# Kernel tuning notes

Measured on AMD Instinct MI355X. Metric: run time of the kernel, lower is better.

## Reference

```python
import jax, jax.numpy as jnp
import numpy as np

N_KNOTS = 10
NEXPERTS = 1
NC = 8
STEP = 1.0 / (N_KNOTS - 1.0)
BN_EPS = 1e-5


def _spline_matrix(n, step):
    # natural cubic spline second-derivative solve matrix (precalc in torch code)
    mat = 4.0 * np.eye(n - 2)
    np.fill_diagonal(mat[1:, :-1], 1.0)
    np.fill_diagonal(mat[:-1, 1:], 1.0)
    A = 6.0 * np.linalg.inv(mat) / step ** 2
    z = np.zeros((1, n - 2))
    A = np.vstack([z, A, z])                      # [n, n-2]
    B = np.zeros((n - 2, n))
    np.fill_diagonal(B, 1.0)
    np.fill_diagonal(B[:, 1:], -2.0)
    np.fill_diagonal(B[:, 2:], 1.0)
    return jnp.asarray(A @ B, dtype=jnp.float32)  # [n, n]


def _conv(x, w, b, stride=2):
    y = jax.lax.conv_general_dilated(x, w, (stride, stride), 'VALID',
                                     dimension_numbers=('NCHW', 'OIHW', 'NCHW'))
    return y + b[None, :, None, None]


def _bn(x, g, be):
    # training-mode batchnorm (module default)
    m = x.mean(axis=(0, 2, 3), keepdims=True)
    v = x.var(axis=(0, 2, 3), keepdims=True)
    return g[None, :, None, None] * (x - m) * jax.lax.rsqrt(v + BN_EPS) + be[None, :, None, None]


def _interpolate(ys, mat):
    # ys: [..., n] -> cubic coeffs a,b,c,d each [..., n-1]
    h = STEP
    M = jnp.einsum('ij,...j->...i', mat, ys)
    a = (M[..., 1:] - M[..., :-1]) / (6.0 * h)
    b = M[..., :-1] / 2.0
    c = (ys[..., 1:] - ys[..., :-1]) / h - (M[..., 1:] + 2.0 * M[..., :-1]) * (h / 6.0)
    d = ys[..., :-1]
    return a, b, c, d


def _apply(coeffs, x):
    # coeffs: 4-tuple each [..., n-1]; x: [..., P] with matching leading dims
    a, b, c, d = coeffs
    xi = jnp.clip(jnp.floor(x / STEP), 0.0, N_KNOTS - 2.0)
    xf = x - xi * STEP
    idx = xi.astype(jnp.int32)
    ag = jnp.take_along_axis(a, idx, axis=-1)
    bg = jnp.take_along_axis(b, idx, axis=-1)
    cg = jnp.take_along_axis(c, idx, axis=-1)
    dg = jnp.take_along_axis(d, idx, axis=-1)
    return ((ag * xf + bg) * xf + cg) * xf + dg


def forward(x, w1, b1, w2, b2, g2, be2, w3, b3, g3, be3, w4, b4, g4, be4,
            w5, b5, g5, be5, fc1_w, fc1_b, fc2_w, fc2_b):
    B, C, H, W = x.shape
    small = x if (H, W) == (256, 256) else jax.image.resize(x, (B, C, 256, 256), 'bilinear')
    h = jax.nn.relu(_conv(small, w1, b1))
    h = _bn(jax.nn.relu(_conv(h, w2, b2)), g2, be2)
    h = _bn(jax.nn.relu(_conv(h, w3, b3)), g3, be3)
    h = _bn(jax.nn.relu(_conv(h, w4, b4)), g4, be4)
    h = _bn(jax.nn.relu(_conv(h, w5, b5)), g5, be5)   # [B, 16nc, 7, 7]
    h = h.mean(axis=(2, 3))                            # avgpool 7 -> [B, 16nc]
    h = jax.nn.relu(h @ fc1_w.T + fc1_b)
    ys = (h @ fc2_w.T + fc2_b).reshape(B, NEXPERTS, 3, N_KNOTS)
    identity = jnp.arange(N_KNOTS, dtype=jnp.float32) / (N_KNOTS - 1.0)
    ysn = ys + identity                                # residual spline
    mat = _spline_matrix(N_KNOTS, STEP)
    coeffs = _interpolate(ysn, mat)                    # each [B,E,3,n-1]
    # per-pixel spline eval at original resolution
    px = jnp.broadcast_to(x.reshape(B, 1, 3, H * W), (B, NEXPERTS, 3, H * W))
    out = _apply(coeffs, px).reshape(B, NEXPERTS, 3, H, W)
    out = jnp.transpose(out, (1, 0, 2, 3, 4))          # [E,B,3,H,W]
    # spline curves sampled at xs = arange(0,1,1/255) (255 points; detached in torch)
    xs = jnp.arange(0.0, 1.0, 1.0 / 255.0, dtype=jnp.float32)
    xs_b = jnp.broadcast_to(xs, (B, NEXPERTS, 3, xs.shape[0]))
    splines = jnp.transpose(_apply(coeffs, xs_b), (1, 0, 2, 3))  # [E,B,3,255]
    return out, splines


def setup_inputs() -> dict:
    key = jax.random.key(0)
    ks = jax.random.split(key, 16)
    n, nc, E = N_KNOTS, NC, NEXPERTS
    d = {}
    d['x'] = jax.random.uniform(ks[0], (8, 3, 1024, 1024), dtype=jnp.float32)
    d['w1'] = jax.random.normal(ks[1], (nc, 3, 3, 3), jnp.float32) * 0.1
    d['b1'] = jnp.zeros((nc,), jnp.float32)
    chans = [nc, 2 * nc, 4 * nc, 8 * nc, 16 * nc]
    for i, (ci, co) in enumerate(zip(chans[:-1], chans[1:]), start=2):
        d[f'w{i}'] = jax.random.normal(ks[i], (co, ci, 3, 3), jnp.float32) * 0.1
        d[f'b{i}'] = jnp.zeros((co,), jnp.float32)
        d[f'g{i}'] = jnp.ones((co,), jnp.float32)
        d[f'be{i}'] = jnp.zeros((co,), jnp.float32)
    d['fc1_w'] = jax.random.normal(ks[10], (16 * nc, 16 * nc), jnp.float32) * 0.05
    d['fc1_b'] = jnp.zeros((16 * nc,), jnp.float32)
    d['fc2_w'] = jax.random.normal(ks[11], (3 * n * E, 16 * nc), jnp.float32) * 0.05
    d['fc2_b'] = jnp.zeros((3 * n * E,), jnp.float32)
    return d


def reference(x, w1, b1, w2, b2, g2, be2, w3, b3, g3, be3, w4, b4, g4, be4,
              w5, b5, g5, be5, fc1_w, fc1_b, fc2_w, fc2_b):
    return forward(x, w1, b1, w2, b2, g2, be2, w3, b3, g3, be3, w4, b4, g4, be4,
                   w5, b5, g5, be5, fc1_w, fc1_b, fc2_w, fc2_b)
```

## Files before the change

### kernel.cpp

```cpp
#include <hip/hip_runtime.h>

#define SPLINE_OFF 25165824
#define STEP_F (1.0f/9.0f)

typedef float f32x4 __attribute__((ext_vector_type(4)));

__global__ __launch_bounds__(256) void resize_k(const float* __restrict__ x,
                                                float* __restrict__ sm,
                                                unsigned* __restrict__ ctr) {
    __shared__ float vs[4][1024];
    const int blk = blockIdx.x;
    const int plane = blk >> 6;
    const int orA = (blk & 63) * 4;
    const int t = threadIdx.x;
    if (blk == 0 && t == 0) ctr[0] = 0u;

    const float W[8] = {0.125f,0.375f,0.625f,0.875f,0.875f,0.625f,0.375f,0.125f};
    const float* p = x + (size_t)plane * 1048576 + t * 4;
    const int rb = 4 * orA - 2;

    float acc[4][4];
    #pragma unroll
    for (int o = 0; o < 4; o++)
        #pragma unroll
        for (int c = 0; c < 4; c++) acc[o][c] = 0.f;

    if (rb >= 0 && rb + 19 <= 1023) {
        #pragma unroll
        for (int k = 0; k < 20; k++) {
            const float4 v = *(const float4*)(p + (size_t)(rb + k) * 1024);
            #pragma unroll
            for (int o = 0; o < 4; o++) {
                const int j = k - 4 * o;
                if (j >= 0 && j < 8) {
                    const float w = W[j] * 0.25f;
                    acc[o][0] = fmaf(v.x, w, acc[o][0]);
                    acc[o][1] = fmaf(v.y, w, acc[o][1]);
                    acc[o][2] = fmaf(v.z, w, acc[o][2]);
                    acc[o][3] = fmaf(v.w, w, acc[o][3]);
                }
            }
        }
    } else {
        #pragma unroll
        for (int o = 0; o < 4; o++) {
            const int r0 = 4 * (orA + o) - 2;
            float bx=0.f,by=0.f,bz=0.f,bw=0.f,wsum=0.f;
            #pragma unroll
            for (int k = 0; k < 8; k++) {
                const int r = r0 + k;
                if (r >= 0 && r < 1024) {
                    const float4 v = *(const float4*)(p + (size_t)r * 1024);
                    bx = fmaf(v.x, W[k], bx); by = fmaf(v.y, W[k], by);
                    bz = fmaf(v.z, W[k], bz); bw = fmaf(v.w, W[k], bw);
                    wsum += W[k];
                }
            }
            const float inv = 1.f / wsum;
            acc[o][0]=bx*inv; acc[o][1]=by*inv; acc[o][2]=bz*inv; acc[o][3]=bw*inv;
        }
    }
    #pragma unroll
    for (int o = 0; o < 4; o++) {
        vs[o][4*t+0]=acc[o][0]; vs[o][4*t+1]=acc[o][1];
        vs[o][4*t+2]=acc[o][2]; vs[o][4*t+3]=acc[o][3];
    }
    __syncthreads();

    const int c0 = 4 * t - 2;
    #pragma unroll
    for (int o = 0; o < 4; o++) {
        float a = 0.f;
        if (c0 >= 0 && c0 + 7 <= 1023) {
            #pragma unroll
            for (int k = 0; k < 8; k++)
                a = fmaf(vs[o][c0 + k], W[k] * 0.25f, a);
        } else {
            float wsum = 0.f;
            #pragma unroll
            for (int k = 0; k < 8; k++) {
                const int c = c0 + k;
                if (c >= 0 && c < 1024) { a = fmaf(vs[o][c], W[k], a); wsum += W[k]; }
            }
            a /= wsum;
        }
        sm[((size_t)plane * 256 + orA + o) * 256 + t] = a;
    }
}

template<int CIN, int COUT, int INW, int OUTW, int CISPLIT, int PIX,
         int NTPREV, int NTOUT, bool INBN, bool STATS, bool WRITE>
__global__ __launch_bounds__(PIX * CISPLIT) void conv_k(
    const float* __restrict__ in, const float* __restrict__ w,
    const float* __restrict__ bias,
    const float* __restrict__ gam, const float* __restrict__ be,
    const float* __restrict__ pS, const float* __restrict__ pQ, float invN,
    float* __restrict__ out,
    float* __restrict__ pSo, float* __restrict__ pQo)
{
    constexpr int BLOCK = PIX * CISPLIT;
    constexpr int CPS = CIN / CISPLIT;
    constexpr int COG = COUT / 2;

    __shared__ float wsm[2][CIN * 9];
    __shared__ float scs[CIN], shs[CIN];
    __shared__ float wrow[2][CIN];
    __shared__ float cadd[2];
    __shared__ float part[CISPLIT][PIX][2];
    __shared__ float red[2][2][PIX / 64];
    __shared__ float sredS[BLOCK], sredQ[BLOCK];

    const int tid = threadIdx.x;
    const int p   = tid & (PIX - 1);
    const int cs  = tid / PIX;
    const int bc  = blockIdx.y;
    const int b   = bc / COG;
    const int co0 = (bc % COG) * 2;

    if constexpr (INBN) {
        constexpr int GRP = BLOCK / CIN;
        constexpr int TERMS = 8 * NTPREV;
        const int ci = tid % CIN;
        const int gi = tid / CIN;
        float s = 0.f, q = 0.f;
        for (int j = gi; j < TERMS; j += GRP) {
            const int bb = j / NTPREV, tl = j - bb * NTPREV;
            const int a = (bb * CIN + ci) * NTPREV + tl;
            s += pS[a]; q += pQ[a];
        }
        sredS[gi * CIN + ci] = s;
        sredQ[gi * CIN + ci] = q;
        __syncthreads();
        if (tid < CIN) {
            float ts = 0.f, tq = 0.f;
            #pragma unroll
            for (int g2 = 0; g2 < GRP; g2++) {
                ts += sredS[g2 * CIN + tid];
                tq += sredQ[g2 * CIN + tid];
            }
            const float m = ts * invN;
            const float v = tq * invN - m * m;
            const float sc = gam[tid] * rsqrtf(v + 1e-5f);
            scs[tid] = sc;
            shs[tid] = be[tid] - m * sc;
        }
        __syncthreads();
    }

    for (int i = tid; i < 2 * CIN * 9; i += BLOCK) {
        const int n = i / (CIN * 9), r = i - n * (CIN * 9), ci = r / 9;
        const float wv = w[(co0 + n) * CIN * 9 + r];
        wsm[n][r] = INBN ? wv * scs[ci] : wv;
    }
    if constexpr (INBN) {
        for (int i = tid; i < 2 * CIN; i += BLOCK) {
            const int n = i / CIN, ci = i - n * CIN;
            const float* wp = w + ((co0 + n) * CIN + ci) * 9;
            float s = 0.f;
            #pragma unroll
            for (int k = 0; k < 9; k++) s += wp[k];
            wrow[n][ci] = s;
        }
    }
    __syncthreads();
    if (tid < 2) {
        float c = bias[co0 + tid];
        if constexpr (INBN) {
            for (int ci = 0; ci < CIN; ci++) c = fmaf(wrow[tid][ci], shs[ci], c);
        }
        cadd[tid] = c;
    }
    __syncthreads();

    const int npix = OUTW * OUTW;
    const int pg = blockIdx.x * PIX + p;
    float a0 = 0.f, a1 = 0.f;
    if (pg < npix) {
        const int oh = pg / OUTW, ow = pg - oh * OUTW;
        const float* ib = in + ((size_t)(b * CIN) + cs * CPS) * (INW * INW)
                             + (size_t)(2 * oh) * INW + 2 * ow;
        #pragma unroll 4
        for (int ci = 0; ci < CPS; ci++) {
            const float* ip = ib + (size_t)ci * (INW * INW);
            const int cw = (cs * CPS + ci) * 9;
            #pragma unroll
            for (int kh = 0; kh < 3; kh++) {
                const float* r = ip + kh * INW;
                #pragma unroll
                for (int kw = 0; kw < 3; kw++) {
                    const float xv = r[kw];
                    a0 = fmaf(xv, wsm[0][cw + kh * 3 + kw], a0);
                    a1 = fmaf(xv, wsm[1][cw + kh * 3 + kw], a1);
                }
            }
        }
    }

    float v0 = 0.f, v1 = 0.f;
    if constexpr (CISPLIT > 1) {
        part[cs][p][0] = a0; part[cs][p][1] = a1;
        __syncthreads();
    }
    if (cs == 0) {
        float s0 = a0, s1 = a1;
        if constexpr (CISPLIT > 1) {
            #pragma unroll
            for (int q = 1; q < CISPLIT; q++) { s0 += part[q][p][0]; s1 += part[q][p][1]; }
        }
        if (pg < npix) {
            v0 = fmaxf(s0 + cadd[0], 0.f);
            v1 = fmaxf(s1 + cadd[1], 0.f);
            if constexpr (WRITE) {
                out[(size_t)(b * COUT + co0) * npix + pg] = v0;
                out[(size_t)(b * COUT + co0 + 1) * npix + pg] = v1;
            }
        }
    }

    if constexpr (STATS) {
        if (cs == 0) {
            float sA = v0, qA = v0 * v0, sB = v1, qB = v1 * v1;
            #pragma unroll
            for (int off = 32; off > 0; off >>= 1) {
                sA += __shfl_down(sA, off); qA += __shfl_down(qA, off);
                sB += __shfl_down(sB, off); qB += __shfl_down(qB, off);
            }
            if ((tid & 63) == 0) {
                red[0][0][tid >> 6] = sA; red[0][1][tid >> 6] = qA;
                red[1][0][tid >> 6] = sB; red[1][1][tid >> 6] = qB;
            }
        }
        __syncthreads();
        if (tid == 0) {
            float tsA = 0.f, tqA = 0.f, tsB = 0.f, tqB = 0.f;
            #pragma unroll
            for (int i = 0; i < PIX / 64; i++) {
                tsA += red[0][0][i]; tqA += red[0][1][i];
                tsB += red[1][0][i]; tqB += red[1][1][i];
            }
            pSo[(b * COUT + co0) * NTOUT + blockIdx.x] = tsA;
            pQo[(b * COUT + co0) * NTOUT + blockIdx.x] = tqA;
            pSo[(b * COUT + co0 + 1) * NTOUT + blockIdx.x] = tsB;
            pQo[(b * COUT + co0 + 1) * NTOUT + blockIdx.x] = tqB;
        }
    }
}

__global__ __launch_bounds__(256) void conv5fc_k(
    const float* __restrict__ in, const float* __restrict__ w,
    const float* __restrict__ bias,
    const float* __restrict__ gam, const float* __restrict__ be,
    const float* __restrict__ pS, const float* __restrict__ pQ,
    float* __restrict__ pS5, float* __restrict__ pQ5,
    const float* __restrict__ g5, const float* __restrict__ be5,
    const float* __restrict__ fc1w, const float* __restrict__ fc1b,
    const float* __restrict__ fc2w, const float* __restrict__ fc2b,
    float* __restrict__ coeff_out, float* __restrict__ splines_out,
    unsigned* __restrict__ ctr)
{
    constexpr int CIN = 64, COUT = 128, INW = 15, OUTW = 7;
    constexpr int CISPLIT = 4, PIX = 64, BLOCK = 256;
    constexpr int CPS = CIN / CISPLIT;
    constexpr int COG = COUT / 2;
    const float invN = 1.0f / 1800.0f;

    __shared__ float wsm[2][CIN * 9];
    __shared__ float scs[CIN], shs[CIN];
    __shared__ float wrow[2][CIN];
    __shared__ float cadd[2];
    __shared__ float part[CISPLIT][PIX][2];
    __shared__ float sredS[BLOCK], sredQ[BLOCK];
    __shared__ unsigned lastFlag;
    __shared__ float fsc5[128], fsh5[128];
    __shared__ float fch[1024], fh1[1024];
    __shared__ float fysn[240];
    __shared__ float fcoef[24][36];

    const int tid = threadIdx.x;
    const int p   = tid & (PIX - 1);
    const int cs  = tid / PIX;
    const int bc  = blockIdx.x;
    const int b   = bc / COG;
    const int co0 = (bc % COG) * 2;

    {
        constexpr int GRP = BLOCK / CIN;
        const int ci = tid % CIN;
        const int gi = tid / CIN;
        float s = 0.f, q = 0.f;
        for (int j = gi; j < 8; j += GRP) {
            const int a = j * CIN + ci;
            s += pS[a]; q += pQ[a];
        }
        sredS[gi * CIN + ci] = s;
        sredQ[gi * CIN + ci] = q;
        __syncthreads();
        if (tid < CIN) {
            float ts = 0.f, tq = 0.f;
            #pragma unroll
            for (int g2 = 0; g2 < GRP; g2++) {
                ts += sredS[g2 * CIN + tid];
                tq += sredQ[g2 * CIN + tid];
            }
            const float m = ts * invN;
            const float v = tq * invN - m * m;
            const float sc = gam[tid] * rsqrtf(v + 1e-5f);
            scs[tid] = sc;
            shs[tid] = be[tid] - m * sc;
        }
        __syncthreads();
    }

    for (int i = tid; i < 2 * CIN * 9; i += BLOCK) {
        const int n = i / (CIN * 9), r = i - n * (CIN * 9), ci = r / 9;
        wsm[n][r] = w[(co0 + n) * CIN * 9 + r] * scs[ci];
    }
    for (int i = tid; i < 2 * CIN; i += BLOCK) {
        const int n = i / CIN, ci = i - n * CIN;
        const float* wp = w + ((co0 + n) * CIN + ci) * 9;
        float s = 0.f;
        #pragma unroll
        for (int k = 0; k < 9; k++) s += wp[k];
        wrow[n][ci] = s;
    }
    __syncthreads();
    if (tid < 2) {
        float c = bias[co0 + tid];
        for (int ci = 0; ci < CIN; ci++) c = fmaf(wrow[tid][ci], shs[ci], c);
        cadd[tid] = c;
    }
    __syncthreads();

    float a0 = 0.f, a1 = 0.f;
    if (p < 49) {
        const int oh = p / OUTW, ow = p - oh * OUTW;
        const float* ib = in + ((size_t)(b * CIN) + cs * CPS) * (INW * INW)
                             + (size_t)(2 * oh) * INW + 2 * ow;
        #pragma unroll 4
        for (int ci = 0; ci < CPS; ci++) {
            const float* ip = ib + (size_t)ci * (INW * INW);
            const int cw = (cs * CPS + ci) * 9;
            #pragma unroll
            for (int kh = 0; kh < 3; kh++) {
                const float* r = ip + kh * INW;
                #pragma unroll
                for (int kw = 0; kw < 3; kw++) {
                    const float xv = r[kw];
                    a0 = fmaf(xv, wsm[0][cw + kh * 3 + kw], a0);
                    a1 = fmaf(xv, wsm[1][cw + kh * 3 + kw], a1);
                }
            }
        }
    }

    part[cs][p][0] = a0; part[cs][p][1] = a1;
    __syncthreads();
    if (cs == 0) {
        float s0 = a0 + part[1][p][0] + part[2][p][0] + part[3][p][0];
        float s1 = a1 + part[1][p][1] + part[2][p][1] + part[3][p][1];
        float v0 = 0.f, v1 = 0.f;
        if (p < 49) {
            v0 = fmaxf(s0 + cadd[0], 0.f);
            v1 = fmaxf(s1 + cadd[1], 0.f);
        }
        float sA = v0, qA = v0 * v0, sB = v1, qB = v1 * v1;
        #pragma unroll
        for (int off = 32; off > 0; off >>= 1) {
            sA += __shfl_down(sA, off); qA += __shfl_down(qA, off);
            sB += __shfl_down(sB, off); qB += __shfl_down(qB, off);
        }
        if (p == 0) {
            pS5[b * COUT + co0] = sA;
            pQ5[b * COUT + co0] = qA;
            pS5[b * COUT + co0 + 1] = sB;
            pQ5[b * COUT + co0 + 1] = qB;
        }
    }
    __syncthreads();

    if (tid == 0) {
        __threadfence();
        unsigned old = atomicAdd(ctr, 1u);
        lastFlag = (old == 511u) ? 1u : 0u;
    }
    __syncthreads();
    if (lastFlag == 0u) return;
    __threadfence();

    const int t = tid;
    if (t < 128) {
        float sv = 0.f, qv = 0.f;
        #pragma unroll
        for (int bb = 0; bb < 8; bb++) { sv += pS5[bb * 128 + t]; qv += pQ5[bb * 128 + t]; }
        float m = sv * (1.f / 392.f);
        float v = qv * (1.f / 392.f) - m * m;
        float sc = g5[t] * rsqrtf(v + 1e-5f);
        fsc5[t] = sc;
        fsh5[t] = be5[t] - m * sc;
    }
    __syncthreads();

    for (int i = t; i < 1024; i += 256) {
        int c = i & 127;
        fch[i] = fmaf(fsc5[c], pS5[i] * (1.f / 49.f), fsh5[c]);
    }
    __syncthreads();

    for (int i = t; i < 1024; i += 256) {
        int bb = i >> 7, j = i & 127;
        float acc = fc1b[j];
        for (int c = 0; c < 128; c++)
            acc = fmaf(fch[(bb << 7) + c], fc1w[(j << 7) + c], acc);
        fh1[i] = fmaxf(acc, 0.f);
    }
    __syncthreads();

    if (t < 240) {
        int bb = t / 30, k = t % 30;
        float acc = fc2b[k];
        for (int j = 0; j < 128; j++)
            acc = fmaf(fh1[(bb << 7) + j], fc2w[(k << 7) + j], acc);
        fysn[t] = acc + (float)(k % 10) * STEP_F;
    }
    __syncthreads();

    if (t < 24) {
        float y[10];
        #pragma unroll
        for (int i = 0; i < 10; i++) y[i] = fysn[t * 10 + i];
        float rhs[9], cp[9], dp[9];
        #pragma unroll
        for (int i = 1; i <= 8; i++)
            rhs[i] = 486.f * (y[i - 1] - 2.f * y[i] + y[i + 1]);
        cp[1] = 0.25f; dp[1] = rhs[1] * 0.25f;
        #pragma unroll
        for (int i = 2; i <= 8; i++) {
            float m = 1.f / (4.f - cp[i - 1]);
            cp[i] = m;
            dp[i] = (rhs[i] - dp[i - 1]) * m;
        }
        float M[10];
        M[0] = 0.f; M[9] = 0.f;
        M[8] = dp[8];
        #pragma unroll
        for (int i = 7; i >= 1; i--) M[i] = dp[i] - cp[i] * M[i + 1];
        #pragma unroll
        for (int i = 0; i < 9; i++) {
            float a = (M[i + 1] - M[i]) * 1.5f;
            float bb2 = M[i] * 0.5f;
            float cc = (y[i + 1] - y[i]) * 9.f - (M[i + 1] + 2.f * M[i]) * (STEP_F / 6.f);
            float dd = y[i];
            fcoef[t][i] = a; fcoef[t][9 + i] = bb2; fcoef[t][18 + i] = cc; fcoef[t][27 + i] = dd;
            coeff_out[t * 36 + i] = a;
            coeff_out[t * 36 + 9 + i] = bb2;
            coeff_out[t * 36 + 18 + i] = cc;
            coeff_out[t * 36 + 27 + i] = dd;
        }
    }
    __syncthreads();

    for (int i = t; i < 24 * 255; i += 256) {
        int bc2 = i / 255, k = i - bc2 * 255;
        float xv = (float)k * (1.0f / 255.0f);
        float xi = floorf(xv * 9.0f);
        xi = fminf(fmaxf(xi, 0.f), 8.f);
        int ix = (int)xi;
        float xf = xv - xi * STEP_F;
        const float* cf = fcoef[bc2];
        splines_out[i] = fmaf(fmaf(fmaf(cf[ix], xf, cf[9 + ix]), xf, cf[18 + ix]), xf, cf[27 + ix]);
    }
}

__global__ __launch_bounds__(256) void apply_k(const float* __restrict__ x,
                                               const float* __restrict__ coeff,
                                               float* __restrict__ out)
{
    __shared__ float cf[36];
    const int blk = blockIdx.x;
    const int plane = blk >> 10;
    const int t = threadIdx.x;
    if (t < 36) cf[t] = coeff[plane * 36 + t];
    __syncthreads();

    size_t base = (size_t)blk * 1024 + (size_t)t * 4;
    float4 v = *(const float4*)(x + base);
    f32x4 o;
    #pragma unroll
    for (int k = 0; k < 4; k++) {
        float xv = (k == 0) ? v.x : (k == 1) ? v.y : (k == 2) ? v.z : v.w;
        float xi = floorf(xv * 9.0f);
        xi = fminf(fmaxf(xi, 0.f), 8.f);
        int ix = (int)xi;
        float xf = xv - xi * STEP_F;
        o[k] = fmaf(fmaf(fmaf(cf[ix], xf, cf[9 + ix]), xf, cf[18 + ix]), xf, cf[27 + ix]);
    }
    __builtin_nontemporal_store(o, (f32x4*)(out + base));
}

extern "C" void kernel_launch(void* const* d_in, const int* in_sizes, int n_in,
                              void* d_out, int out_size, void* d_ws, size_t ws_size,
                              hipStream_t stream) {
    (void)in_sizes; (void)n_in; (void)out_size; (void)ws_size;

    const float* x    = (const float*)d_in[0];
    const float* w1   = (const float*)d_in[1];
    const float* b1   = (const float*)d_in[2];
    const float* w2   = (const float*)d_in[3];
    const float* b2   = (const float*)d_in[4];
    const float* g2   = (const float*)d_in[5];
    const float* be2  = (const float*)d_in[6];
    const float* w3   = (const float*)d_in[7];
    const float* b3   = (const float*)d_in[8];
    const float* g3   = (const float*)d_in[9];
    const float* be3  = (const float*)d_in[10];
    const float* w4   = (const float*)d_in[11];
    const float* b4   = (const float*)d_in[12];
    const float* g4   = (const float*)d_in[13];
    const float* be4  = (const float*)d_in[14];
    const float* w5   = (const float*)d_in[15];
    const float* b5   = (const float*)d_in[16];
    const float* g5   = (const float*)d_in[17];
    const float* be5  = (const float*)d_in[18];
    const float* fc1w = (const float*)d_in[19];
    const float* fc1b = (const float*)d_in[20];
    const float* fc2w = (const float*)d_in[21];
    const float* fc2b = (const float*)d_in[22];

    float* out = (float*)d_out;
    float* wsf = (float*)d_ws;

    float* pS2 = wsf + 0;
    float* pQ2 = wsf + 2048;
    float* pS3 = wsf + 4096;
    float* pQ3 = wsf + 5120;
    float* pS4 = wsf + 6144;
    float* pQ4 = wsf + 6656;
    float* pS5 = wsf + 7168;
    float* pQ5 = wsf + 8192;
    float* coeff = wsf + 9216;
    unsigned* ctr = (unsigned*)(wsf + 10240);

    float* sm  = out;
    float* h1  = out + 1572864;
    float* h2  = out + 2605120;
    float* h3  = out + 3113152;
    float* h4  = out + 3359168;

    resize_k<<<1536, 256, 0, stream>>>(x, sm, ctr);

    conv_k<3, 8, 256, 127, 1, 256, 1, 1, false, false, true>
        <<<dim3(64, 32), 256, 0, stream>>>(sm, w1, b1, nullptr, nullptr,
                                           nullptr, nullptr, 0.f,
                                           h1, nullptr, nullptr);
    conv_k<8, 16, 127, 63, 1, 256, 1, 16, false, true, true>
        <<<dim3(16, 64), 256, 0, stream>>>(h1, w2, b2, nullptr, nullptr,
                                           nullptr, nullptr, 0.f,
                                           h2, pS2, pQ2);
    conv_k<16, 32, 63, 31, 1, 256, 16, 4, true, true, true>
        <<<dim3(4, 128), 256, 0, stream>>>(h2, w3, b3, g2, be2,
                                           pS2, pQ2, 1.0f / 31752.0f,
                                           h3, pS3, pQ3);
    conv_k<32, 64, 31, 15, 2, 256, 4, 1, true, true, true>
        <<<dim3(1, 256), 512, 0, stream>>>(h3, w4, b4, g3, be3,
                                           pS3, pQ3, 1.0f / 7688.0f,
                                           h4, pS4, pQ4);
    conv5fc_k<<<512, 256, 0, stream>>>(h4, w5, b5, g4, be4,
                                       pS4, pQ4, pS5, pQ5,
                                       g5, be5, fc1w, fc1b, fc2w, fc2b,
                                       coeff, out + SPLINE_OFF, ctr);

    apply_k<<<24576, 256, 0, stream>>>(x, coeff, out);
}
```

Measured before the change: 130.5 us.

## Fuse conv1 and conv2 into one tiled kernel with shared-memory intermediate

Replaces the separate conv1 and conv2 launches with one kernel that computes each 8x8 output tile of conv2. It first computes the needed 17x17 conv1 patch for all 8 channels into shared memory, then conv2, and emits per-tile batchnorm partial sums. This removes the h1 global round trip and one launch. The cost is recomputing overlapping halo pixels of conv1 and having fewer blocks (512) with more shared memory each. The conv3 stats partial count changes to 64 per plane, and the workspace layout is enlarged to match.

```diff
diff --git a/kernel.cpp b/kernel.cpp
--- a/kernel.cpp
+++ b/kernel.cpp
@@ -85,6 +85,100 @@
             a /= wsum;
         }
         sm[((size_t)plane * 256 + orA + o) * 256 + t] = a;
+    }
+}
+
+__global__ __launch_bounds__(256) void c1c2_k(
+    const float* __restrict__ sm,
+    const float* __restrict__ w1, const float* __restrict__ b1,
+    const float* __restrict__ w2, const float* __restrict__ b2,
+    float* __restrict__ h2, float* __restrict__ pS2, float* __restrict__ pQ2)
+{
+    __shared__ float smT[3 * 1225];
+    __shared__ float c1T[8 * 289];
+    __shared__ float w1s[216];
+    __shared__ float w2s[1152];
+    __shared__ float bs[24];
+
+    const int tile = blockIdx.x;
+    const int b    = blockIdx.y;
+    const int tx = tile & 7, ty = tile >> 3;
+    const int R0 = ty * 8, C0 = tx * 8;
+    const int t = threadIdx.x;
+
+    if (t < 216) w1s[t] = w1[t];
+    for (int i = t; i < 1152; i += 256) w2s[i] = w2[i];
+    if (t < 8) bs[t] = b1[t];
+    else if (t < 24) bs[t] = b2[t - 8];
+
+    const int r0 = 4 * R0, c0 = 4 * C0;
+    for (int i = t; i < 3675; i += 256) {
+        const int ch = i / 1225, rem = i - ch * 1225;
+        const int r = rem / 35, c = rem - r * 35;
+        const int gr = r0 + r, gc = c0 + c;
+        float v = 0.f;
+        if (gr < 256 && gc < 256)
+            v = sm[((size_t)(b * 3 + ch) << 16) + (gr << 8) + gc];
+        smT[i] = v;
+    }
+    __syncthreads();
+
+    for (int i = t; i < 2312; i += 256) {
+        const int co = i / 289, pp = i - co * 289;
+        const int r = pp / 17, c = pp - r * 17;
+        float acc = bs[co];
+        #pragma unroll
+        for (int ch = 0; ch < 3; ch++) {
+            const float* sp = &smT[ch * 1225 + (2 * r) * 35 + 2 * c];
+            const float* wp = &w1s[co * 27 + ch * 9];
+            #pragma unroll
+            for (int kh = 0; kh < 3; kh++) {
+                acc = fmaf(sp[kh * 35 + 0], wp[kh * 3 + 0], acc);
+                acc = fmaf(sp[kh * 35 + 1], wp[kh * 3 + 1], acc);
+                acc = fmaf(sp[kh * 35 + 2], wp[kh * 3 + 2], acc);
+            }
+        }
+        c1T[i] = fmaxf(acc, 0.f);
+    }
+    __syncthreads();
+
+    const int px = t & 63, cog = t >> 6;
+    const int pr = px >> 3, pc = px & 7;
+    const bool valid = (R0 + pr < 63) && (C0 + pc < 63);
+    float vals[4];
+    #pragma unroll
+    for (int k = 0; k < 4; k++) {
+        const int co = cog * 4 + k;
+        float acc = bs[8 + co];
+        #pragma unroll
+        for (int ci = 0; ci < 8; ci++) {
+            const float* cp = &c1T[ci * 289 + (2 * pr) * 17 + 2 * pc];
+            const float* wp = &w2s[co * 72 + ci * 9];
+            #pragma unroll
+            for (int kh = 0; kh < 3; kh++) {
+                acc = fmaf(cp[kh * 17 + 0], wp[kh * 3 + 0], acc);
+                acc = fmaf(cp[kh * 17 + 1], wp[kh * 3 + 1], acc);
+                acc = fmaf(cp[kh * 17 + 2], wp[kh * 3 + 2], acc);
+            }
+        }
+        const float v = valid ? fmaxf(acc, 0.f) : 0.f;
+        vals[k] = v;
+        if (valid)
+            h2[(size_t)(b * 16 + co) * 3969 + (R0 + pr) * 63 + (C0 + pc)] = v;
+    }
+    #pragma unroll
+    for (int k = 0; k < 4; k++) {
+        float s = vals[k], q = vals[k] * vals[k];
+        #pragma unroll
+        for (int off = 32; off > 0; off >>= 1) {
+            s += __shfl_down(s, off);
+            q += __shfl_down(q, off);
+        }
+        if (px == 0) {
+            const int co = cog * 4 + k;
+            pS2[(b * 16 + co) * 64 + tile] = s;
+            pQ2[(b * 16 + co) * 64 + tile] = q;
+        }
     }
 }
 
@@ -530,33 +624,26 @@
     float* wsf = (float*)d_ws;
 
     float* pS2 = wsf + 0;
-    float* pQ2 = wsf + 2048;
-    float* pS3 = wsf + 4096;
-    float* pQ3 = wsf + 5120;
-    float* pS4 = wsf + 6144;
-    float* pQ4 = wsf + 6656;
-    float* pS5 = wsf + 7168;
-    float* pQ5 = wsf + 8192;
-    float* coeff = wsf + 9216;
-    unsigned* ctr = (unsigned*)(wsf + 10240);
+    float* pQ2 = wsf + 8192;
+    float* pS3 = wsf + 16384;
+    float* pQ3 = wsf + 17408;
+    float* pS4 = wsf + 18432;
+    float* pQ4 = wsf + 18944;
+    float* pS5 = wsf + 19456;
+    float* pQ5 = wsf + 20480;
+    float* coeff = wsf + 21504;
+    unsigned* ctr = (unsigned*)(wsf + 22400);
 
     float* sm  = out;
-    float* h1  = out + 1572864;
-    float* h2  = out + 2605120;
-    float* h3  = out + 3113152;
-    float* h4  = out + 3359168;
+    float* h2  = out + 1572864;
+    float* h3  = out + 2080896;
+    float* h4  = out + 2326912;
 
     resize_k<<<1536, 256, 0, stream>>>(x, sm, ctr);
 
-    conv_k<3, 8, 256, 127, 1, 256, 1, 1, false, false, true>
-        <<<dim3(64, 32), 256, 0, stream>>>(sm, w1, b1, nullptr, nullptr,
-                                           nullptr, nullptr, 0.f,
-                                           h1, nullptr, nullptr);
-    conv_k<8, 16, 127, 63, 1, 256, 1, 16, false, true, true>
-        <<<dim3(16, 64), 256, 0, stream>>>(h1, w2, b2, nullptr, nullptr,
-                                           nullptr, nullptr, 0.f,
-                                           h2, pS2, pQ2);
-    conv_k<16, 32, 63, 31, 1, 256, 16, 4, true, true, true>
+    c1c2_k<<<dim3(64, 8), 256, 0, stream>>>(sm, w1, b1, w2, b2, h2, pS2, pQ2);
+
+    conv_k<16, 32, 63, 31, 1, 256, 64, 4, true, true, true>
         <<<dim3(4, 128), 256, 0, stream>>>(h2, w3, b3, g2, be2,
                                            pS2, pQ2, 1.0f / 31752.0f,
                                            h3, pS3, pQ3);
```

Result: slower. 151.9 us (+16.4%).

## Fuse conv3, conv4 and conv5+FC into one persistent kernel with grid barriers

Applied to the files above, without the earlier changes.

Replaces three separate launches (conv3, conv4, conv5fc) with a single 512-block kernel. The stages are separated by software grid-wide barriers built on atomic counters, which are reset in the resize kernel. The goal is to remove kernel launch gaps and tail effects on these small late stages. The trade-off is that conv4 now runs with 256 threads and a different tiling (2 tiles of 128 pixels). Correctness also relies on all 512 blocks being co-resident for the spin barrier to avoid deadlock.

```diff
diff --git a/kernel.cpp b/kernel.cpp
--- a/kernel.cpp
+++ b/kernel.cpp
@@ -13,7 +13,7 @@
     const int plane = blk >> 6;
     const int orA = (blk & 63) * 4;
     const int t = threadIdx.x;
-    if (blk == 0 && t == 0) ctr[0] = 0u;
+    if (blk == 0 && t < 3) ctr[t] = 0u;
 
     const float W[8] = {0.125f,0.375f,0.625f,0.875f,0.875f,0.625f,0.375f,0.125f};
     const float* p = x + (size_t)plane * 1048576 + t * 4;
@@ -246,11 +246,183 @@
     }
 }
 
-__global__ __launch_bounds__(256) void conv5fc_k(
+struct S345 {
+    float wsm[2][576];
+    float scs[64], shs[64];
+    float wrow[2][64];
+    float cadd[2];
+    float part[512];
+    float red[2][2][4];
+    float sredS[256], sredQ[256];
+};
+
+__device__ __forceinline__ void gb_sync(unsigned* cnt, unsigned target) {
+    __syncthreads();
+    if (threadIdx.x == 0) {
+        __threadfence();
+        __hip_atomic_fetch_add(cnt, 1u, __ATOMIC_RELAXED, __HIP_MEMORY_SCOPE_AGENT);
+        while (__hip_atomic_load(cnt, __ATOMIC_RELAXED, __HIP_MEMORY_SCOPE_AGENT) < target)
+            __builtin_amdgcn_s_sleep(2);
+        __threadfence();
+    }
+    __syncthreads();
+}
+
+template<int CIN, int COUT, int INW, int OUTW, int CISPLIT, int PIX,
+         int NTPREV, int NTOUT, bool WRITE>
+__device__ __forceinline__ void phase345(
+    S345& s,
     const float* __restrict__ in, const float* __restrict__ w,
-    const float* __restrict__ bias,
-    const float* __restrict__ gam, const float* __restrict__ be,
-    const float* __restrict__ pS, const float* __restrict__ pQ,
+    const float* __restrict__ bias, const float* __restrict__ gam,
+    const float* __restrict__ be, const float* __restrict__ pS,
+    const float* __restrict__ pQ, float invN,
+    float* __restrict__ out, float* __restrict__ pSo, float* __restrict__ pQo,
+    int bid, int tid)
+{
+    constexpr int BLOCK = 256;
+    constexpr int CPS = CIN / CISPLIT;
+    constexpr int COG = COUT / 2;
+    const int p    = tid & (PIX - 1);
+    const int cs   = tid / PIX;
+    const int tile = bid % NTOUT;
+    const int bc   = bid / NTOUT;
+    const int b    = bc / COG;
+    const int co0  = (bc % COG) * 2;
+
+    {
+        constexpr int GRP = BLOCK / CIN;
+        constexpr int TERMS = 8 * NTPREV;
+        const int ci = tid % CIN;
+        const int gi = tid / CIN;
+        float sv = 0.f, qv = 0.f;
+        for (int j = gi; j < TERMS; j += GRP) {
+            const int bb = j / NTPREV, tl = j - bb * NTPREV;
+            const int a = (bb * CIN + ci) * NTPREV + tl;
+            sv += pS[a]; qv += pQ[a];
+        }
+        s.sredS[gi * CIN + ci] = sv;
+        s.sredQ[gi * CIN + ci] = qv;
+        __syncthreads();
+        if (tid < CIN) {
+            float ts = 0.f, tq = 0.f;
+            #pragma unroll
+            for (int g2 = 0; g2 < GRP; g2++) {
+                ts += s.sredS[g2 * CIN + tid];
+                tq += s.sredQ[g2 * CIN + tid];
+            }
+            const float m = ts * invN;
+            const float v = tq * invN - m * m;
+            const float sc = gam[tid] * rsqrtf(v + 1e-5f);
+            s.scs[tid] = sc;
+            s.shs[tid] = be[tid] - m * sc;
+        }
+        __syncthreads();
+    }
+
+    for (int i = tid; i < 2 * CIN * 9; i += BLOCK) {
+        const int n = i / (CIN * 9), r = i - n * (CIN * 9), ci = r / 9;
+        s.wsm[n][r] = w[(co0 + n) * CIN * 9 + r] * s.scs[ci];
+    }
+    for (int i = tid; i < 2 * CIN; i += BLOCK) {
+        const int n = i / CIN, ci = i - n * CIN;
+        const float* wp = w + ((co0 + n) * CIN + ci) * 9;
+        float sv = 0.f;
+        #pragma unroll
+        for (int k = 0; k < 9; k++) sv += wp[k];
+        s.wrow[n][ci] = sv;
+    }
+    __syncthreads();
+    if (tid < 2) {
+        float c = bias[co0 + tid];
+        for (int ci = 0; ci < CIN; ci++) c = fmaf(s.wrow[tid][ci], s.shs[ci], c);
+        s.cadd[tid] = c;
+    }
+    __syncthreads();
+
+    const int npix = OUTW * OUTW;
+    const int pg = tile * PIX + p;
+    float a0 = 0.f, a1 = 0.f;
+    if (pg < npix) {
+        const int oh = pg / OUTW, ow = pg - oh * OUTW;
+        const float* ib = in + ((size_t)(b * CIN) + cs * CPS) * (INW * INW)
+                             + (size_t)(2 * oh) * INW + 2 * ow;
+        #pragma unroll 4
+        for (int ci = 0; ci < CPS; ci++) {
+            const float* ip = ib + (size_t)ci * (INW * INW);
+            const int cw = (cs * CPS + ci) * 9;
+            #pragma unroll
+            for (int kh = 0; kh < 3; kh++) {
+                const float* r = ip + kh * INW;
+                #pragma unroll
+                for (int kw = 0; kw < 3; kw++) {
+                    const float xv = r[kw];
+                    a0 = fmaf(xv, s.wsm[0][cw + kh * 3 + kw], a0);
+                    a1 = fmaf(xv, s.wsm[1][cw + kh * 3 + kw], a1);
+                }
+            }
+        }
+    }
+
+    float v0 = 0.f, v1 = 0.f;
+    if constexpr (CISPLIT > 1) {
+        s.part[(cs * PIX + p) * 2 + 0] = a0;
+        s.part[(cs * PIX + p) * 2 + 1] = a1;
+        __syncthreads();
+    }
+    if (cs == 0) {
+        float s0 = a0, s1 = a1;
+        if constexpr (CISPLIT > 1) {
+            #pragma unroll
+            for (int q = 1; q < CISPLIT; q++) {
+                s0 += s.part[(q * PIX + p) * 2 + 0];
+                s1 += s.part[(q * PIX + p) * 2 + 1];
+            }
+        }
+        if (pg < npix) {
+            v0 = fmaxf(s0 + s.cadd[0], 0.f);
+            v1 = fmaxf(s1 + s.cadd[1], 0.f);
+            if constexpr (WRITE) {
+                out[(size_t)(b * COUT + co0) * npix + pg] = v0;
+                out[(size_t)(b * COUT + co0 + 1) * npix + pg] = v1;
+            }
+        }
+        float sA = v0, qA = v0 * v0, sB = v1, qB = v1 * v1;
+        #pragma unroll
+        for (int off = 32; off > 0; off >>= 1) {
+            sA += __shfl_down(sA, off); qA += __shfl_down(qA, off);
+            sB += __shfl_down(sB, off); qB += __shfl_down(qB, off);
+        }
+        if ((tid & 63) == 0) {
+            s.red[0][0][tid >> 6] = sA; s.red[0][1][tid >> 6] = qA;
+            s.red[1][0][tid >> 6] = sB; s.red[1][1][tid >> 6] = qB;
+        }
+    }
+    __syncthreads();
+    if (tid == 0) {
+        float tsA = 0.f, tqA = 0.f, tsB = 0.f, tqB = 0.f;
+        #pragma unroll
+        for (int i = 0; i < PIX / 64; i++) {
+            tsA += s.red[0][0][i]; tqA += s.red[0][1][i];
+            tsB += s.red[1][0][i]; tqB += s.red[1][1][i];
+        }
+        pSo[(b * COUT + co0) * NTOUT + tile] = tsA;
+        pQo[(b * COUT + co0) * NTOUT + tile] = tqA;
+        pSo[(b * COUT + co0 + 1) * NTOUT + tile] = tsB;
+        pQo[(b * COUT + co0 + 1) * NTOUT + tile] = tqB;
+    }
+}
+
+__global__ __launch_bounds__(256) void c345_k(
+    const float* __restrict__ h2,
+    const float* __restrict__ w3, const float* __restrict__ b3,
+    const float* __restrict__ g2, const float* __restrict__ be2,
+    const float* __restrict__ pS2, const float* __restrict__ pQ2,
+    float* __restrict__ h3, float* __restrict__ pS3, float* __restrict__ pQ3,
+    const float* __restrict__ w4, const float* __restrict__ b4,
+    const float* __restrict__ g3, const float* __restrict__ be3,
+    float* __restrict__ h4, float* __restrict__ pS4, float* __restrict__ pQ4,
+    const float* __restrict__ w5, const float* __restrict__ b5,
+    const float* __restrict__ g4, const float* __restrict__ be4,
     float* __restrict__ pS5, float* __restrict__ pQ5,
     const float* __restrict__ g5, const float* __restrict__ be5,
     const float* __restrict__ fc1w, const float* __restrict__ fc1b,
@@ -258,129 +430,34 @@
     float* __restrict__ coeff_out, float* __restrict__ splines_out,
     unsigned* __restrict__ ctr)
 {
-    constexpr int CIN = 64, COUT = 128, INW = 15, OUTW = 7;
-    constexpr int CISPLIT = 4, PIX = 64, BLOCK = 256;
-    constexpr int CPS = CIN / CISPLIT;
-    constexpr int COG = COUT / 2;
-    const float invN = 1.0f / 1800.0f;
-
-    __shared__ float wsm[2][CIN * 9];
-    __shared__ float scs[CIN], shs[CIN];
-    __shared__ float wrow[2][CIN];
-    __shared__ float cadd[2];
-    __shared__ float part[CISPLIT][PIX][2];
-    __shared__ float sredS[BLOCK], sredQ[BLOCK];
+    __shared__ S345 s;
     __shared__ unsigned lastFlag;
     __shared__ float fsc5[128], fsh5[128];
     __shared__ float fch[1024], fh1[1024];
     __shared__ float fysn[240];
     __shared__ float fcoef[24][36];
 
+    const int bid = blockIdx.x;
     const int tid = threadIdx.x;
-    const int p   = tid & (PIX - 1);
-    const int cs  = tid / PIX;
-    const int bc  = blockIdx.x;
-    const int b   = bc / COG;
-    const int co0 = (bc % COG) * 2;
-
-    {
-        constexpr int GRP = BLOCK / CIN;
-        const int ci = tid % CIN;
-        const int gi = tid / CIN;
-        float s = 0.f, q = 0.f;
-        for (int j = gi; j < 8; j += GRP) {
-            const int a = j * CIN + ci;
-            s += pS[a]; q += pQ[a];
-        }
-        sredS[gi * CIN + ci] = s;
-        sredQ[gi * CIN + ci] = q;
-        __syncthreads();
-        if (tid < CIN) {
-            float ts = 0.f, tq = 0.f;
-            #pragma unroll
-            for (int g2 = 0; g2 < GRP; g2++) {
-                ts += sredS[g2 * CIN + tid];
-                tq += sredQ[g2 * CIN + tid];
-            }
-            const float m = ts * invN;
-            const float v = tq * invN - m * m;
-            const float sc = gam[tid] * rsqrtf(v + 1e-5f);
-            scs[tid] = sc;
-            shs[tid] = be[tid] - m * sc;
-        }
-        __syncthreads();
-    }
-
-    for (int i = tid; i < 2 * CIN * 9; i += BLOCK) {
-        const int n = i / (CIN * 9), r = i - n * (CIN * 9), ci = r / 9;
-        wsm[n][r] = w[(co0 + n) * CIN * 9 + r] * scs[ci];
-    }
-    for (int i = tid; i < 2 * CIN; i += BLOCK) {
-        const int n = i / CIN, ci = i - n * CIN;
-        const float* wp = w + ((co0 + n) * CIN + ci) * 9;
-        float s = 0.f;
-        #pragma unroll
-        for (int k = 0; k < 9; k++) s += wp[k];
-        wrow[n][ci] = s;
-    }
-    __syncthreads();
-    if (tid < 2) {
-        float c = bias[co0 + tid];
-        for (int ci = 0; ci < CIN; ci++) c = fmaf(wrow[tid][ci], shs[ci], c);
-        cadd[tid] = c;
-    }
-    __syncthreads();
-
-    float a0 = 0.f, a1 = 0.f;
-    if (p < 49) {
-        const int oh = p / OUTW, ow = p - oh * OUTW;
-        const float* ib = in + ((size_t)(b * CIN) + cs * CPS) * (INW * INW)
-                             + (size_t)(2 * oh) * INW + 2 * ow;
-        #pragma unroll 4
-        for (int ci = 0; ci < CPS; ci++) {
-            const float* ip = ib + (size_t)ci * (INW * INW);
-            const int cw = (cs * CPS + ci) * 9;
-            #pragma unroll
-            for (int kh = 0; kh < 3; kh++) {
-                const float* r = ip + kh * INW;
-                #pragma unroll
-                for (int kw = 0; kw < 3; kw++) {
-                    const float xv = r[kw];
-                    a0 = fmaf(xv, wsm[0][cw + kh * 3 + kw], a0);
-                    a1 = fmaf(xv, wsm[1][cw + kh * 3 + kw], a1);
-                }
-            }
-        }
-    }
-
-    part[cs][p][0] = a0; part[cs][p][1] = a1;
-    __syncthreads();
-    if (cs == 0) {
-        float s0 = a0 + part[1][p][0] + part[2][p][0] + part[3][p][0];
-        float s1 = a1 + part[1][p][1] + part[2][p][1] + part[3][p][1];
-        float v0 = 0.f, v1 = 0.f;
-        if (p < 49) {
-            v0 = fmaxf(s0 + cadd[0], 0.f);
-            v1 = fmaxf(s1 + cadd[1], 0.f);
-        }
-        float sA = v0, qA = v0 * v0, sB = v1, qB = v1 * v1;
-        #pragma unroll
-        for (int off = 32; off > 0; off >>= 1) {
-            sA += __shfl_down(sA, off); qA += __shfl_down(qA, off);
-            sB += __shfl_down(sB, off); qB += __shfl_down(qB, off);
-        }
-        if (p == 0) {
-            pS5[b * COUT + co0] = sA;
-            pQ5[b * COUT + co0] = qA;
-            pS5[b * COUT + co0 + 1] = sB;
-            pQ5[b * COUT + co0 + 1] = qB;
-        }
-    }
-    __syncthreads();
-
+
+    phase345<16, 32, 63, 31, 1, 256, 16, 4, true>(
+        s, h2, w3, b3, g2, be2, pS2, pQ2, 1.0f / 31752.0f,
+        h3, pS3, pQ3, bid, tid);
+    gb_sync(&ctr[0], 512u);
+
+    phase345<32, 64, 31, 15, 2, 128, 4, 2, true>(
+        s, h3, w4, b4, g3, be3, pS3, pQ3, 1.0f / 7688.0f,
+        h4, pS4, pQ4, bid, tid);
+    gb_sync(&ctr[1], 512u);
+
+    phase345<64, 128, 15, 7, 4, 64, 2, 1, false>(
+        s, h4, w5, b5, g4, be4, pS4, pQ4, 1.0f / 1800.0f,
+        nullptr, pS5, pQ5, bid, tid);
+
+    __syncthreads();
     if (tid == 0) {
         __threadfence();
-        unsigned old = atomicAdd(ctr, 1u);
+        unsigned old = atomicAdd(&ctr[2], 1u);
         lastFlag = (old == 511u) ? 1u : 0u;
     }
     __syncthreads();
@@ -534,11 +611,11 @@
     float* pS3 = wsf + 4096;
     float* pQ3 = wsf + 5120;
     float* pS4 = wsf + 6144;
-    float* pQ4 = wsf + 6656;
-    float* pS5 = wsf + 7168;
-    float* pQ5 = wsf + 8192;
-    float* coeff = wsf + 9216;
-    unsigned* ctr = (unsigned*)(wsf + 10240);
+    float* pQ4 = wsf + 7168;
+    float* pS5 = wsf + 8192;
+    float* pQ5 = wsf + 9216;
+    float* coeff = wsf + 10240;
+    unsigned* ctr = (unsigned*)(wsf + 11264);
 
     float* sm  = out;
     float* h1  = out + 1572864;
@@ -556,18 +633,15 @@
         <<<dim3(16, 64), 256, 0, stream>>>(h1, w2, b2, nullptr, nullptr,
                                            nullptr, nullptr, 0.f,
                                            h2, pS2, pQ2);
-    conv_k<16, 32, 63, 31, 1, 256, 16, 4, true, true, true>
-        <<<dim3(4, 128), 256, 0, stream>>>(h2, w3, b3, g2, be2,
-                                           pS2, pQ2, 1.0f / 31752.0f,
-                                           h3, pS3, pQ3);
-    conv_k<32, 64, 31, 15, 2, 256, 4, 1, true, true, true>
-        <<<dim3(1, 256), 512, 0, stream>>>(h3, w4, b4, g3, be3,
-                                           pS3, pQ3, 1.0f / 7688.0f,
-                                           h4, pS4, pQ4);
-    conv5fc_k<<<512, 256, 0, stream>>>(h4, w5, b5, g4, be4,
-                                       pS4, pQ4, pS5, pQ5,
-                                       g5, be5, fc1w, fc1b, fc2w, fc2b,
-                                       coeff, out + SPLINE_OFF, ctr);
+    c345_k<<<512, 256, 0, stream>>>(h2,
+                                    w3, b3, g2, be2, pS2, pQ2,
+                                    h3, pS3, pQ3,
+                                    w4, b4, g3, be3,
+                                    h4, pS4, pQ4,
+                                    w5, b5, g4, be4,
+                                    pS5, pQ5,
+                                    g5, be5, fc1w, fc1b, fc2w, fc2b,
+                                    coeff, out + SPLINE_OFF, ctr);
 
     apply_k<<<24576, 256, 0, stream>>>(x, coeff, out);
 }
```

Measured after the change: 199.8 us. 53.0% more time.
